# Optimization experiments

Measured on AMD Instinct MI355X. Metric: run time of the kernel, lower is better.

Reference implementation:

```python
import jax, jax.numpy as jnp
import numpy as np

VOCAB = 256
EMBED = 128
HIDDEN = 512
BATCH = 64
SEQ = 1024


def setup_inputs() -> dict:
    key = jax.random.key(0)
    ks = jax.random.split(key, 6)
    x = jax.random.randint(ks[0], (BATCH, SEQ), 0, VOCAB)
    hidden = jnp.zeros((BATCH, HIDDEN), dtype=jnp.float32)
    embedding = jax.random.normal(ks[1], (VOCAB, EMBED), dtype=jnp.float32)
    W_xh = jax.random.normal(ks[2], (EMBED, HIDDEN), dtype=jnp.float32) * 0.01
    W_hh = jax.random.normal(ks[3], (HIDDEN, HIDDEN), dtype=jnp.float32) * 0.01
    b_h = jnp.zeros((HIDDEN,), dtype=jnp.float32)
    # nn.Linear(hidden, vocab): weight [vocab, hidden], bias [vocab]
    W_hy_w = jax.random.normal(ks[4], (VOCAB, HIDDEN), dtype=jnp.float32) * (1.0 / np.sqrt(HIDDEN))
    W_hy_b = jax.random.normal(ks[5], (VOCAB,), dtype=jnp.float32) * 0.01
    return {"x": x, "hidden": hidden, "embedding": embedding, "W_xh": W_xh,
            "W_hh": W_hh, "b_h": b_h, "W_hy_w": W_hy_w, "W_hy_b": W_hy_b}


def reference(x, hidden, embedding, W_xh, W_hh, b_h, W_hy_w, W_hy_b):
    # x: [b, l] int tokens -> embed: [b, l, e]
    x_embed = embedding[x]
    # Precompute input projections in one batched GEMM: [l, b, h]
    xw = jnp.einsum('ble,eh->lbh', x_embed, W_xh) + b_h

    def step(h, xw_t):
        h_new = jnp.tanh(xw_t + h @ W_hh)
        return h_new, h_new

    final_hidden, outs = jax.lax.scan(step, hidden, xw)  # outs: [l, b, h]
    outs = jnp.transpose(outs, (1, 0, 2))  # [b, l, h]
    logits = outs @ W_hy_w.T + W_hy_b  # [b, l, vocab]
    return logits, final_hidden
```

## Files before the change

### kernel.cpp

```cpp
#include <hip/hip_runtime.h>
#include <hip/hip_bf16.h>
#include <stdint.h>

#define BATCH  64
#define SEQ    1024
#define EMBED  128
#define HIDDEN 512
#define VOCAB  256

using bf16 = __hip_bfloat16;
typedef __attribute__((ext_vector_type(8))) short bf16x8;
typedef __attribute__((ext_vector_type(4))) float f32x4;

__device__ __forceinline__ float bfu(unsigned short u) {
    return __uint_as_float(((unsigned)u) << 16);
}

__global__ void k_cvt(const float* __restrict__ in, bf16* __restrict__ out, int n) {
    int i = blockIdx.x * 256 + threadIdx.x;
    if (i < n) out[i] = __float2bfloat16(in[i]);
}

__global__ void k_txp_wxh(const float* __restrict__ in, bf16* __restrict__ out) {
    int idx = blockIdx.x * 256 + threadIdx.x;
    int e = idx >> 9, j = idx & 511;
    out[j * EMBED + e] = __float2bfloat16(in[idx]);
}

__global__ void k_txp_whh(const float* __restrict__ in, bf16* __restrict__ out) {
    int idx = blockIdx.x * 256 + threadIdx.x;
    int k = idx >> 9, n = idx & 511;
    out[n * HIDDEN + k] = __float2bfloat16(in[idx]);
}

template<bool GATHER, bool OUT_BF16, bool PERMUTE>
__global__ __launch_bounds__(256) void k_gemm(
    const bf16* __restrict__ A,
    const int*  __restrict__ xtok,
    const bf16* __restrict__ B,
    const float* __restrict__ bias,
    float* __restrict__ Cf,
    bf16*  __restrict__ Cb,
    int M, int N, int K)
{
    __shared__ bf16 As[64][72];
    __shared__ bf16 Bs[64][72];
    const int m0 = blockIdx.x * 64, n0 = blockIdx.y * 64;
    const int tid  = threadIdx.x;
    const int lane = tid & 63, wid = tid >> 6;
    const int wm = wid >> 1, wn = wid & 1;
    const int lrow = tid >> 3, lc8 = tid & 7;

    f32x4 acc[2][2] = {};

    for (int k0 = 0; k0 < K; k0 += 64) {
#pragma unroll
        for (int pass = 0; pass < 2; ++pass) {
            int row = pass * 32 + lrow;
            const bf16* asrc;
            if (GATHER) {
                int m = m0 + row;
                int t = m >> 6, bb = m & 63;
                int tok = xtok[bb * SEQ + t];
                asrc = A + (size_t)tok * K + k0 + lc8 * 8;
            } else {
                asrc = A + (size_t)(m0 + row) * K + k0 + lc8 * 8;
            }
            *reinterpret_cast<uint4*>(&As[row][lc8 * 8]) = *reinterpret_cast<const uint4*>(asrc);
            *reinterpret_cast<uint4*>(&Bs[row][lc8 * 8]) =
                *reinterpret_cast<const uint4*>(B + (size_t)(n0 + row) * K + k0 + lc8 * 8);
        }
        __syncthreads();
#pragma unroll
        for (int kk = 0; kk < 2; ++kk) {
            bf16x8 af[2], bg[2];
#pragma unroll
            for (int mt = 0; mt < 2; ++mt)
                af[mt] = *reinterpret_cast<const bf16x8*>(
                    &As[wm * 32 + mt * 16 + (lane & 15)][kk * 32 + (lane >> 4) * 8]);
#pragma unroll
            for (int nt = 0; nt < 2; ++nt)
                bg[nt] = *reinterpret_cast<const bf16x8*>(
                    &Bs[wn * 32 + nt * 16 + (lane & 15)][kk * 32 + (lane >> 4) * 8]);
#pragma unroll
            for (int mt = 0; mt < 2; ++mt)
#pragma unroll
                for (int nt = 0; nt < 2; ++nt)
                    acc[mt][nt] = __builtin_amdgcn_mfma_f32_16x16x32_bf16(
                        af[mt], bg[nt], acc[mt][nt], 0, 0, 0);
        }
        __syncthreads();
    }
    if (PERMUTE) {
        const int t = m0 >> 6, wid_s = n0 >> 6;
#pragma unroll
        for (int mt = 0; mt < 2; ++mt) {
            int blk = wm * 2 + mt;
            bf16 tmp[8];
#pragma unroll
            for (int nt = 0; nt < 2; ++nt) {
                int col = n0 + wn * 32 + nt * 16 + (lane & 15);
                float bv = bias[col];
#pragma unroll
                for (int r = 0; r < 4; ++r)
                    tmp[nt * 4 + r] = __float2bfloat16(acc[mt][nt][r] + bv);
            }
            size_t off = (((size_t)(t * 4 + blk) * 512) + wid_s * 64 + lane) * 16 + wn * 8;
            *reinterpret_cast<uint4*>(Cb + off) = *reinterpret_cast<uint4*>(tmp);
        }
    } else {
#pragma unroll
        for (int mt = 0; mt < 2; ++mt) {
            int rbase = m0 + wm * 32 + mt * 16 + (lane >> 4) * 4;
#pragma unroll
            for (int nt = 0; nt < 2; ++nt) {
                int col = n0 + wn * 32 + nt * 16 + (lane & 15);
                float bv = bias[col];
#pragma unroll
                for (int r = 0; r < 4; ++r) {
                    float v = acc[mt][nt][r] + bv;
                    size_t off = (size_t)(rbase + r) * N + col;
                    if (OUT_BF16) Cb[off] = __float2bfloat16(v);
                    else          Cf[off] = v;
                }
            }
        }
    }
}

#define ROWS 16
#define CHK_LDS 3
#define CHK_REG 8
#define WRES_STRIDE (CHK_LDS * 32 + 8)
#define H_STRIDE (HIDDEN + 8)

__global__ __launch_bounds__(512, 2) void k_scan_mfma(
    const bf16* __restrict__ xwp,
    const bf16* __restrict__ wt,
    const float* __restrict__ h0,
    bf16* __restrict__ hh,
    float* __restrict__ hfin)
{
    __shared__ bf16 wres[HIDDEN * WRES_STRIDE];
    __shared__ bf16 h_lds[2][ROWS * H_STRIDE];

    const int tid  = threadIdx.x;
    const int lane = tid & 63, wid = tid >> 6;
    const int b0   = blockIdx.x * ROWS;
    const int scol = wid * 64;
    const int lm   = lane & 15, lk = lane >> 4;

    {
        const bf16* src = wt + (size_t)tid * HIDDEN;
        bf16* dst = &wres[tid * WRES_STRIDE];
#pragma unroll
        for (int j = 0; j < (CHK_LDS * 32) / 8; ++j)
            *reinterpret_cast<uint4*>(dst + j * 8) =
                *reinterpret_cast<const uint4*>(src + j * 8);
    }
    {
        int row = tid >> 5, c = (tid & 31) * 16;
        const float* src = h0 + (size_t)(b0 + row) * HIDDEN + c;
        bf16 tmp[16];
#pragma unroll
        for (int j = 0; j < 16; ++j) tmp[j] = __float2bfloat16(src[j]);
        *reinterpret_cast<uint4*>(&h_lds[0][row * H_STRIDE + c])     = *reinterpret_cast<uint4*>(&tmp[0]);
        *reinterpret_cast<uint4*>(&h_lds[0][row * H_STRIDE + c + 8]) = *reinterpret_cast<uint4*>(&tmp[8]);
    }

    bf16x8 breg[CHK_REG][4];
#pragma unroll
    for (int c = 0; c < CHK_REG; ++c)
#pragma unroll
        for (int nt = 0; nt < 4; ++nt) {
            breg[c][nt] = *reinterpret_cast<const bf16x8*>(
                wt + (size_t)(scol + nt * 16 + lm) * HIDDEN + (CHK_LDS + c) * 32 + lk * 8);
            asm volatile("" : "+v"(breg[c][nt]));
        }

    const bf16* grow[4];
    const bf16* lrowp[4];
#pragma unroll
    for (int nt = 0; nt < 4; ++nt) {
        int row = scol + nt * 16 + lm;
        grow[nt]  = wt + (size_t)row * HIDDEN + lk * 8;
        lrowp[nt] = &wres[row * WRES_STRIDE + lk * 8];
    }

    const int srow = tid >> 5, sc = (tid & 31) * 16;

    __syncthreads();

    int p = 0;
    for (int t = 0; t < SEQ; ++t) {
        if (t > 0) {
            uint4 v0 = *reinterpret_cast<const uint4*>(&h_lds[p][srow * H_STRIDE + sc]);
            uint4 v1 = *reinterpret_cast<const uint4*>(&h_lds[p][srow * H_STRIDE + sc + 8]);
            bf16* dst = hh + ((size_t)(b0 + srow) * SEQ + (t - 1)) * HIDDEN + sc;
            *reinterpret_cast<uint4*>(dst)     = v0;
            *reinterpret_cast<uint4*>(dst + 8) = v1;
        }

        ushort xe[16];
        {
            const uint4* xp = reinterpret_cast<const uint4*>(xwp) +
                              ((size_t)(t * 4 + blockIdx.x) * 512 + tid) * 2;
            *reinterpret_cast<uint4*>(&xe[0]) = xp[0];
            *reinterpret_cast<uint4*>(&xe[8]) = xp[1];
        }

        f32x4 acc[4] = {};
#pragma unroll
        for (int kc = 0; kc < 16; ++kc) {
            bf16x8 af = *reinterpret_cast<const bf16x8*>(
                &h_lds[p][lm * H_STRIDE + kc * 32 + lk * 8]);
#pragma unroll
            for (int nt = 0; nt < 4; ++nt) {
                bf16x8 bg;
                if (kc < CHK_LDS)
                    bg = *reinterpret_cast<const bf16x8*>(lrowp[nt] + kc * 32);
                else if (kc < CHK_LDS + CHK_REG)
                    bg = breg[kc - CHK_LDS][nt];
                else
                    bg = *reinterpret_cast<const bf16x8*>(grow[nt] + kc * 32);
                acc[nt] = __builtin_amdgcn_mfma_f32_16x16x32_bf16(af, bg, acc[nt], 0, 0, 0);
            }
        }

#pragma unroll
        for (int nt = 0; nt < 4; ++nt) {
            int col = scol + nt * 16 + lm;
#pragma unroll
            for (int r = 0; r < 4; ++r) {
                int m = lk * 4 + r;
                float pre = acc[nt][r] + bfu(xe[nt * 4 + r]);
                float e2  = __expf(2.f * pre);
                float hn  = 1.f - 2.f / (e2 + 1.f);
                h_lds[p ^ 1][m * H_STRIDE + col] = __float2bfloat16(hn);
                if (t == SEQ - 1) hfin[(size_t)(b0 + m) * HIDDEN + col] = hn;
            }
        }
        p ^= 1;
        __syncthreads();
    }

    {
        uint4 v0 = *reinterpret_cast<const uint4*>(&h_lds[p][srow * H_STRIDE + sc]);
        uint4 v1 = *reinterpret_cast<const uint4*>(&h_lds[p][srow * H_STRIDE + sc + 8]);
        bf16* dst = hh + ((size_t)(b0 + srow) * SEQ + (SEQ - 1)) * HIDDEN + sc;
        *reinterpret_cast<uint4*>(dst)     = v0;
        *reinterpret_cast<uint4*>(dst + 8) = v1;
    }
}

extern "C" void kernel_launch(void* const* d_in, const int* in_sizes, int n_in,
                              void* d_out, int out_size, void* d_ws, size_t ws_size,
                              hipStream_t stream) {
    const int*   x    = (const int*)  d_in[0];
    const float* h0   = (const float*)d_in[1];
    const float* emb  = (const float*)d_in[2];
    const float* wxh  = (const float*)d_in[3];
    const float* whh  = (const float*)d_in[4];
    const float* bh   = (const float*)d_in[5];
    const float* whyw = (const float*)d_in[6];
    const float* whyb = (const float*)d_in[7];

    float* logits = (float*)d_out;
    float* hfin   = logits + (size_t)BATCH * SEQ * VOCAB;

    char* p = (char*)d_ws;
    bf16* xwp    = (bf16*)p; p += (size_t)SEQ * BATCH * HIDDEN * 2;
    bf16* hh     = (bf16*)p; p += (size_t)BATCH * SEQ * HIDDEN * 2;
    bf16* wt     = (bf16*)p; p += (size_t)HIDDEN * HIDDEN * 2;
    bf16* wxh_t  = (bf16*)p; p += (size_t)HIDDEN * EMBED * 2;
    bf16* emb_bf = (bf16*)p; p += (size_t)VOCAB * EMBED * 2;
    bf16* why_bf = (bf16*)p; p += (size_t)VOCAB * HIDDEN * 2;

    k_txp_whh<<<(HIDDEN * HIDDEN + 255) / 256, 256, 0, stream>>>(whh, wt);
    k_cvt<<<(VOCAB * EMBED + 255) / 256, 256, 0, stream>>>(emb, emb_bf, VOCAB * EMBED);
    k_cvt<<<(VOCAB * HIDDEN + 255) / 256, 256, 0, stream>>>(whyw, why_bf, VOCAB * HIDDEN);
    k_txp_wxh<<<(EMBED * HIDDEN + 255) / 256, 256, 0, stream>>>(wxh, wxh_t);

    k_gemm<true, true, true><<<dim3((SEQ * BATCH) / 64, HIDDEN / 64), 256, 0, stream>>>(
        emb_bf, x, wxh_t, bh, nullptr, xwp, SEQ * BATCH, HIDDEN, EMBED);

    k_scan_mfma<<<BATCH / ROWS, 512, 0, stream>>>(xwp, wt, h0, hh, hfin);

    k_gemm<false, false, false><<<dim3((BATCH * SEQ) / 64, VOCAB / 64), 256, 0, stream>>>(
        hh, nullptr, why_bf, whyb, logits, nullptr, BATCH * SEQ, VOCAB, HIDDEN);
}
```

Measured before the change: 3.299 ms.

## Split recurrent scan across 16 waves with 32 columns each

The scan kernel now runs 1024 threads per block instead of 512, and each wave owns 32 hidden columns instead of 64. This halves the per-wave MFMA chain and the register-resident weight slice on the latency-bound sequential path. The input-projection GEMM's permuted output layout is changed to match the new per-thread xw fetch of 8 values. The cost is more waves contending on the per-step barrier and on the shared h reads.

```diff
diff --git a/kernel.cpp b/kernel.cpp
--- a/kernel.cpp
+++ b/kernel.cpp
@@ -92,7 +92,8 @@
         __syncthreads();
     }
     if (PERMUTE) {
-        const int t = m0 >> 6, wid_s = n0 >> 6;
+        const int t = m0 >> 6;
+        const int wid_s = (n0 >> 5) + wn;
 #pragma unroll
         for (int mt = 0; mt < 2; ++mt) {
             int blk = wm * 2 + mt;
@@ -105,7 +106,8 @@
                 for (int r = 0; r < 4; ++r)
                     tmp[nt * 4 + r] = __float2bfloat16(acc[mt][nt][r] + bv);
             }
-            size_t off = (((size_t)(t * 4 + blk) * 512) + wid_s * 64 + lane) * 16 + wn * 8;
+            size_t off = ((size_t)(t * 4 + blk) * 1024 +
+                          wid_s * 64 + (lane >> 4) * 16 + (lane & 15)) * 8;
             *reinterpret_cast<uint4*>(Cb + off) = *reinterpret_cast<uint4*>(tmp);
         }
     } else {
@@ -134,7 +136,7 @@
 #define WRES_STRIDE (CHK_LDS * 32 + 8)
 #define H_STRIDE (HIDDEN + 8)
 
-__global__ __launch_bounds__(512, 2) void k_scan_mfma(
+__global__ __launch_bounds__(1024, 4) void k_scan_mfma(
     const bf16* __restrict__ xwp,
     const bf16* __restrict__ wt,
     const float* __restrict__ h0,
@@ -147,47 +149,48 @@
     const int tid  = threadIdx.x;
     const int lane = tid & 63, wid = tid >> 6;
     const int b0   = blockIdx.x * ROWS;
-    const int scol = wid * 64;
+    const int scol = wid * 32;
     const int lm   = lane & 15, lk = lane >> 4;
 
     {
-        const bf16* src = wt + (size_t)tid * HIDDEN;
-        bf16* dst = &wres[tid * WRES_STRIDE];
-#pragma unroll
-        for (int j = 0; j < (CHK_LDS * 32) / 8; ++j)
+        int row = tid >> 1, half = tid & 1;
+        const bf16* src = wt + (size_t)row * HIDDEN + half * 48;
+        bf16* dst = &wres[row * WRES_STRIDE + half * 48];
+#pragma unroll
+        for (int j = 0; j < 6; ++j)
             *reinterpret_cast<uint4*>(dst + j * 8) =
                 *reinterpret_cast<const uint4*>(src + j * 8);
     }
     {
-        int row = tid >> 5, c = (tid & 31) * 16;
+        int row = tid >> 6, c = (tid & 63) * 8;
         const float* src = h0 + (size_t)(b0 + row) * HIDDEN + c;
-        bf16 tmp[16];
-#pragma unroll
-        for (int j = 0; j < 16; ++j) tmp[j] = __float2bfloat16(src[j]);
-        *reinterpret_cast<uint4*>(&h_lds[0][row * H_STRIDE + c])     = *reinterpret_cast<uint4*>(&tmp[0]);
-        *reinterpret_cast<uint4*>(&h_lds[0][row * H_STRIDE + c + 8]) = *reinterpret_cast<uint4*>(&tmp[8]);
-    }
-
-    bf16x8 breg[CHK_REG][4];
+        bf16 tmp[8];
+#pragma unroll
+        for (int j = 0; j < 8; ++j) tmp[j] = __float2bfloat16(src[j]);
+        *reinterpret_cast<uint4*>(&h_lds[0][row * H_STRIDE + c]) =
+            *reinterpret_cast<uint4*>(&tmp[0]);
+    }
+
+    bf16x8 breg[CHK_REG][2];
 #pragma unroll
     for (int c = 0; c < CHK_REG; ++c)
 #pragma unroll
-        for (int nt = 0; nt < 4; ++nt) {
+        for (int nt = 0; nt < 2; ++nt) {
             breg[c][nt] = *reinterpret_cast<const bf16x8*>(
                 wt + (size_t)(scol + nt * 16 + lm) * HIDDEN + (CHK_LDS + c) * 32 + lk * 8);
             asm volatile("" : "+v"(breg[c][nt]));
         }
 
-    const bf16* grow[4];
-    const bf16* lrowp[4];
-#pragma unroll
-    for (int nt = 0; nt < 4; ++nt) {
+    const bf16* grow[2];
+    const bf16* lrowp[2];
+#pragma unroll
+    for (int nt = 0; nt < 2; ++nt) {
         int row = scol + nt * 16 + lm;
         grow[nt]  = wt + (size_t)row * HIDDEN + lk * 8;
         lrowp[nt] = &wres[row * WRES_STRIDE + lk * 8];
     }
 
-    const int srow = tid >> 5, sc = (tid & 31) * 16;
+    const int srow = tid >> 6, sc = (tid & 63) * 8;
 
     __syncthreads();
 
@@ -195,27 +198,22 @@
     for (int t = 0; t < SEQ; ++t) {
         if (t > 0) {
             uint4 v0 = *reinterpret_cast<const uint4*>(&h_lds[p][srow * H_STRIDE + sc]);
-            uint4 v1 = *reinterpret_cast<const uint4*>(&h_lds[p][srow * H_STRIDE + sc + 8]);
             bf16* dst = hh + ((size_t)(b0 + srow) * SEQ + (t - 1)) * HIDDEN + sc;
-            *reinterpret_cast<uint4*>(dst)     = v0;
-            *reinterpret_cast<uint4*>(dst + 8) = v1;
-        }
-
-        ushort xe[16];
-        {
-            const uint4* xp = reinterpret_cast<const uint4*>(xwp) +
-                              ((size_t)(t * 4 + blockIdx.x) * 512 + tid) * 2;
-            *reinterpret_cast<uint4*>(&xe[0]) = xp[0];
-            *reinterpret_cast<uint4*>(&xe[8]) = xp[1];
-        }
-
-        f32x4 acc[4] = {};
+            *reinterpret_cast<uint4*>(dst) = v0;
+        }
+
+        ushort xe[8];
+        *reinterpret_cast<uint4*>(&xe[0]) =
+            *(reinterpret_cast<const uint4*>(xwp) +
+              (size_t)(t * 4 + blockIdx.x) * 1024 + tid);
+
+        f32x4 acc[2] = {};
 #pragma unroll
         for (int kc = 0; kc < 16; ++kc) {
             bf16x8 af = *reinterpret_cast<const bf16x8*>(
                 &h_lds[p][lm * H_STRIDE + kc * 32 + lk * 8]);
 #pragma unroll
-            for (int nt = 0; nt < 4; ++nt) {
+            for (int nt = 0; nt < 2; ++nt) {
                 bf16x8 bg;
                 if (kc < CHK_LDS)
                     bg = *reinterpret_cast<const bf16x8*>(lrowp[nt] + kc * 32);
@@ -228,7 +226,7 @@
         }
 
 #pragma unroll
-        for (int nt = 0; nt < 4; ++nt) {
+        for (int nt = 0; nt < 2; ++nt) {
             int col = scol + nt * 16 + lm;
 #pragma unroll
             for (int r = 0; r < 4; ++r) {
@@ -246,10 +244,8 @@
 
     {
         uint4 v0 = *reinterpret_cast<const uint4*>(&h_lds[p][srow * H_STRIDE + sc]);
-        uint4 v1 = *reinterpret_cast<const uint4*>(&h_lds[p][srow * H_STRIDE + sc + 8]);
         bf16* dst = hh + ((size_t)(b0 + srow) * SEQ + (SEQ - 1)) * HIDDEN + sc;
-        *reinterpret_cast<uint4*>(dst)     = v0;
-        *reinterpret_cast<uint4*>(dst + 8) = v1;
+        *reinterpret_cast<uint4*>(dst) = v0;
     }
 }
 
@@ -284,7 +280,7 @@
     k_gemm<true, true, true><<<dim3((SEQ * BATCH) / 64, HIDDEN / 64), 256, 0, stream>>>(
         emb_bf, x, wxh_t, bh, nullptr, xwp, SEQ * BATCH, HIDDEN, EMBED);
 
-    k_scan_mfma<<<BATCH / ROWS, 512, 0, stream>>>(xwp, wt, h0, hh, hfin);
+    k_scan_mfma<<<BATCH / ROWS, 1024, 0, stream>>>(xwp, wt, h0, hh, hfin);
 
     k_gemm<false, false, false><<<dim3((BATCH * SEQ) / 64, VOCAB / 64), 256, 0, stream>>>(
         hh, nullptr, why_bf, whyb, logits, nullptr, BATCH * SEQ, VOCAB, HIDDEN);
```

New measurement: 2.939 ms. -10.9%, faster.
